# Optimization experiments

Hardware: AMD Instinct MI355X
Metric: run time of the kernel (lower is better)

Reference implementation:

```python
import jax, jax.numpy as jnp
import numpy as np

B, S, DIM = 2, 2048, 4096
NH, NKV, HD = 32, 8, 128
RANK, ALPHA = 16, 32
THETA = 500000.0
SCALE = ALPHA / RANK  # 2.0


def setup_inputs() -> dict:
    key = jax.random.key(0)
    ks = jax.random.split(key, 14)
    s = 0.02  # init scale for numerical stability
    inp = {
        "x": jax.random.normal(ks[0], (B, S, DIM), jnp.float32),
        "w_q": jax.random.normal(ks[1], (NH * HD, DIM), jnp.float32) * s,
        "w_k": jax.random.normal(ks[2], (NKV * HD, DIM), jnp.float32) * s,
        "w_v": jax.random.normal(ks[3], (NKV * HD, DIM), jnp.float32) * s,
        "w_o": jax.random.normal(ks[4], (DIM, NH * HD), jnp.float32) * s,
        "lora_wq_a": jax.random.normal(ks[5], (RANK, DIM), jnp.float32) * s,
        "lora_wq_b": jax.random.normal(ks[6], (NH * HD, RANK), jnp.float32) * s,
        "lora_wk_a": jax.random.normal(ks[7], (RANK, DIM), jnp.float32) * s,
        "lora_wk_b": jax.random.normal(ks[8], (NKV * HD, RANK), jnp.float32) * s,
        "lora_wv_a": jax.random.normal(ks[9], (RANK, DIM), jnp.float32) * s,
        "lora_wv_b": jax.random.normal(ks[10], (NKV * HD, RANK), jnp.float32) * s,
        "lora_wo_a": jax.random.normal(ks[11], (RANK, DIM), jnp.float32) * s,
        "lora_wo_b": jax.random.normal(ks[12], (DIM, RANK), jnp.float32) * s,
        "cache_k": jnp.zeros((B, S, NKV, HD), jnp.float32),
        "cache_v": jnp.zeros((B, S, NKV, HD), jnp.float32),
    }
    # rotary frequencies: freqs_cis = exp(i * t * theta^{-2j/hd}), shape (S, HD//2)
    inv_freq = 1.0 / (THETA ** (np.arange(0, HD, 2, dtype=np.float32) / HD))
    t = np.arange(S, dtype=np.float32)
    freqs = np.outer(t, inv_freq)
    inp["freqs_cos"] = jnp.asarray(np.cos(freqs))
    inp["freqs_sin"] = jnp.asarray(np.sin(freqs))
    # causal mask (prefill)
    inp["mask"] = jnp.triu(jnp.full((S, S), -1e9, jnp.float32), 1)
    inp["start_pos"] = 0
    return inp


def _apply_rope(t, cos, sin):
    # t: [b, s, h, d]; cos/sin: [s, d//2] -> complex rotation on (even, odd) pairs
    b, s, h, d = t.shape
    t2 = t.reshape(b, s, h, d // 2, 2)
    tr, ti = t2[..., 0], t2[..., 1]
    c = cos[None, :, None, :]
    sn = sin[None, :, None, :]
    out = jnp.stack([tr * c - ti * sn, tr * sn + ti * c], axis=-1)
    return out.reshape(b, s, h, d)


def reference(x, w_q, w_k, w_v, w_o,
              lora_wq_a, lora_wq_b, lora_wk_a, lora_wk_b,
              lora_wv_a, lora_wv_b, lora_wo_a, lora_wo_b,
              cache_k, cache_v, freqs_cos, freqs_sin, mask, start_pos):
    bsz, seqlen, _ = x.shape
    n_rep = NH // NKV

    xq = x @ w_q.T + SCALE * ((x @ lora_wq_a.T) @ lora_wq_b.T)
    xk = x @ w_k.T + SCALE * ((x @ lora_wk_a.T) @ lora_wk_b.T)
    xv = x @ w_v.T + SCALE * ((x @ lora_wv_a.T) @ lora_wv_b.T)

    xq = xq.reshape(bsz, seqlen, NH, HD)
    xk = xk.reshape(bsz, seqlen, NKV, HD)
    xv = xv.reshape(bsz, seqlen, NKV, HD)

    xq = _apply_rope(xq, freqs_cos, freqs_sin)
    xk = _apply_rope(xk, freqs_cos, freqs_sin)

    # KV-cache write + read of [:start_pos+seqlen]
    cache_k = jax.lax.dynamic_update_slice(cache_k, xk, (0, start_pos, 0, 0))
    cache_v = jax.lax.dynamic_update_slice(cache_v, xv, (0, start_pos, 0, 0))
    kv_len = start_pos + seqlen
    keys = cache_k[:, :kv_len]      # [b, k, nkv, hd]
    values = cache_v[:, :kv_len]

    # GQA expansion (repeat_interleave on head axis)
    keys = jnp.repeat(keys, n_rep, axis=2)    # [b, k, nh, hd]
    values = jnp.repeat(values, n_rep, axis=2)

    scores = jnp.einsum("bqhd,bkhd->bhqk", xq, keys) / jnp.sqrt(jnp.float32(HD))
    scores = scores + mask[None, None, :, :]
    probs = jax.nn.softmax(scores.astype(jnp.float32), axis=-1).astype(xq.dtype)
    out = jnp.einsum("bhqk,bkhd->bqhd", probs, values).reshape(bsz, seqlen, NH * HD)

    # NOTE: the original applies the output LoRA to x (not to out) -- kept faithful.
    return out @ w_o.T + SCALE * ((x @ lora_wo_a.T) @ lora_wo_b.T)
```

## Files before the change

### kernel.cpp

```cpp
#include <hip/hip_runtime.h>


typedef __attribute__((ext_vector_type(8))) short short8;
typedef __attribute__((ext_vector_type(4))) short short4v;
typedef __attribute__((ext_vector_type(4))) float f32x4;

#define LORA_SCALE 2.0f
#define INV_SQRT_HD 0.08838834764831845f

static __device__ __forceinline__ unsigned short f2bf(float f) {
  union { float f; unsigned int u; } v; v.f = f;
  unsigned int r = (v.u + 0x7fffu + ((v.u >> 16) & 1u)) >> 16;
  return (unsigned short)r;
}
static __device__ __forceinline__ float bf2f(unsigned short h) {
  union { unsigned int u; float f; } v; v.u = ((unsigned int)h) << 16;
  return v.f;
}

#define GL16(src, dst) __builtin_amdgcn_global_load_lds( \
    (const unsigned int __attribute__((address_space(1)))*)(src), \
    (unsigned int __attribute__((address_space(3)))*)(dst), 16, 0, 0)

#define VMC4() asm volatile("s_waitcnt vmcnt(4)" ::: "memory")
#define VMC0() asm volatile("s_waitcnt vmcnt(0)" ::: "memory")
#define BARX() __builtin_amdgcn_s_barrier()

template <int BF16OUT>
__global__ __launch_bounds__(512, 2) void gemm256_kernel(
    const unsigned short* __restrict__ A,
    const unsigned short* __restrict__ B,
    void* __restrict__ C, int K, int ldc, int T)
{
  __shared__ unsigned short As[2][2][8192];
  __shared__ unsigned short Bs[2][2][8192];
  const int tid = threadIdx.x;
  const int w = tid >> 6, l = tid & 63;
  const int l15 = l & 15, lhi = l >> 4;
  const int gx = gridDim.x;
  const int flat = blockIdx.y * gx + blockIdx.x;
  const int chunk = (gx * gridDim.y) >> 3;
  const int swz = (flat & 7) * chunk + (flat >> 3);
  const int m0 = (swz / gx) * 256, n0 = (swz % gx) * 256;
  const int wm = (w >> 2) * 128, wn = (w & 3) * 64;

  const f32x4 vz = {0.f, 0.f, 0.f, 0.f};
  f32x4 acc[8][4];
#pragma unroll
  for (int i = 0; i < 8; ++i)
#pragma unroll
    for (int j = 0; j < 4; ++j) acc[i][j] = vz;

  const int srow = tid >> 2, sg = tid & 3;
  const int sgsw = sg ^ ((tid >> 3) & 3);
  const unsigned short* gA = A + (size_t)(m0 + srow) * K + sgsw * 8;
  const unsigned short* gB = B + (size_t)(n0 + srow) * K + sgsw * 8;
  const size_t rK = (size_t)128 * K;
  const int ld0 = srow * 32 + sg * 8;

#define STAGE_A(buf, kh, kb) do { \
    GL16(gA + (kb) + (kh) * 32, &As[buf][kh][ld0]); \
    GL16(gA + rK + (kb) + (kh) * 32, &As[buf][kh][4096 + ld0]); } while (0)
#define STAGE_B(buf, kh, kb) do { \
    GL16(gB + (kb) + (kh) * 32, &Bs[buf][kh][ld0]); \
    GL16(gB + rK + (kb) + (kh) * 32, &Bs[buf][kh][4096 + ld0]); } while (0)
#define LDA8(buf, kc) do { \
    _Pragma("unroll") for (int mi = 0; mi < 8; ++mi) { \
      int r = wm + mi * 16 + l15; \
      af[mi] = *(const short8*)&As[buf][kc][r * 32 + ((lhi ^ ((r >> 1) & 3)) << 3)]; } } while (0)
#define LDB1(buf, kc, ni) \
    (*(const short8*)&Bs[buf][kc][(wn + (ni) * 16 + l15) * 32 + \
        ((lhi ^ (((wn + (ni) * 16 + l15) >> 1) & 3)) << 3)])
#define MM16(bx, by, cx, cy) do { \
    __builtin_amdgcn_s_setprio(1); \
    _Pragma("unroll") for (int mi = 0; mi < 8; ++mi) { \
      acc[mi][cx] = __builtin_amdgcn_mfma_f32_16x16x32_bf16(af[mi], bx, acc[mi][cx], 0, 0, 0); \
      acc[mi][cy] = __builtin_amdgcn_mfma_f32_16x16x32_bf16(af[mi], by, acc[mi][cy], 0, 0, 0); } \
    __builtin_amdgcn_s_setprio(0); } while (0)

  STAGE_A(0, 0, 0); STAGE_B(0, 0, 0); STAGE_A(0, 1, 0); STAGE_B(0, 1, 0);
  VMC4(); BARX();

  short8 af[8], b0, b1, b2, b3;
  for (int t = 0; t < T - 1; ++t) {
    const int cur = t & 1, nxt = cur ^ 1;
    const int kb = (t + 1) * 64;
    LDA8(cur, 0);
    b0 = LDB1(cur, 0, 0); b1 = LDB1(cur, 0, 1);
    STAGE_A(nxt, 0, kb);
    MM16(b0, b1, 0, 1);
    b2 = LDB1(cur, 0, 2); b3 = LDB1(cur, 0, 3);
    STAGE_B(nxt, 0, kb);
    VMC4(); BARX();
    MM16(b2, b3, 2, 3);
    LDA8(cur, 1);
    b0 = LDB1(cur, 1, 0); b1 = LDB1(cur, 1, 1);
    STAGE_A(nxt, 1, kb);
    MM16(b0, b1, 0, 1);
    b2 = LDB1(cur, 1, 2); b3 = LDB1(cur, 1, 3);
    STAGE_B(nxt, 1, kb);
    VMC4(); BARX();
    MM16(b2, b3, 2, 3);
  }
  {
    const int cur = (T - 1) & 1;
    LDA8(cur, 0);
    b0 = LDB1(cur, 0, 0); b1 = LDB1(cur, 0, 1);
    MM16(b0, b1, 0, 1);
    b2 = LDB1(cur, 0, 2); b3 = LDB1(cur, 0, 3);
    VMC0(); BARX();
    MM16(b2, b3, 2, 3);
    LDA8(cur, 1);
    b0 = LDB1(cur, 1, 0); b1 = LDB1(cur, 1, 1);
    MM16(b0, b1, 0, 1);
    b2 = LDB1(cur, 1, 2); b3 = LDB1(cur, 1, 3);
    MM16(b2, b3, 2, 3);
  }
#pragma unroll
  for (int mi = 0; mi < 8; ++mi)
#pragma unroll
    for (int ni = 0; ni < 4; ++ni)
#pragma unroll
      for (int j = 0; j < 4; ++j) {
        size_t row = (size_t)(m0 + wm + mi * 16 + lhi * 4 + j);
        size_t col = (size_t)(n0 + wn + ni * 16 + l15);
        if (BF16OUT) ((unsigned short*)C)[row * ldc + col] = f2bf(acc[mi][ni][j]);
        else         ((float*)C)[row * ldc + col] = acc[mi][ni][j];
      }
#undef STAGE_A
#undef STAGE_B
#undef LDA8
#undef LDB1
#undef MM16
}

template <int BF16OUT>
__global__ __launch_bounds__(512, 2) void gemm256b_kernel(
    const unsigned short* __restrict__ A,
    const unsigned short* __restrict__ B,
    void* __restrict__ C, int K, int ldc, int T)
{
  __shared__ unsigned short As[2][8192];
  __shared__ unsigned short Bs[2][8192];
  const int tid = threadIdx.x;
  const int w = tid >> 6, l = tid & 63;
  const int l15 = l & 15, lhi = l >> 4;
  const int gx = gridDim.x;
  const int flat = blockIdx.y * gx + blockIdx.x;
  const int chunk = (gx * gridDim.y) >> 3;
  const int swz = (flat & 7) * chunk + (flat >> 3);
  const int m0 = (swz / gx) * 256, n0 = (swz % gx) * 256;
  const int wm = (w >> 2) * 128, wn = (w & 3) * 64;

  const f32x4 vz = {0.f, 0.f, 0.f, 0.f};
  f32x4 acc[8][4];
#pragma unroll
  for (int i = 0; i < 8; ++i)
#pragma unroll
    for (int j = 0; j < 4; ++j) acc[i][j] = vz;

  const int srow = tid >> 2, sg = tid & 3;
  const int sgsw = sg ^ ((tid >> 3) & 3);
  const unsigned short* gA = A + (size_t)(m0 + srow) * K + sgsw * 8;
  const unsigned short* gB = B + (size_t)(n0 + srow) * K + sgsw * 8;
  const size_t rK = (size_t)128 * K;
  const int ld0 = srow * 32 + sg * 8;

#define STAGE_AB(buf, kb) do { \
    GL16(gA + (kb), &As[buf][ld0]); \
    GL16(gA + rK + (kb), &As[buf][4096 + ld0]); \
    GL16(gB + (kb), &Bs[buf][ld0]); \
    GL16(gB + rK + (kb), &Bs[buf][4096 + ld0]); } while (0)
#define LDA8(buf) do { \
    _Pragma("unroll") for (int mi = 0; mi < 8; ++mi) { \
      int r = wm + mi * 16 + l15; \
      af[mi] = *(const short8*)&As[buf][r * 32 + ((lhi ^ ((r >> 1) & 3)) << 3)]; } } while (0)
#define LDB1(buf, ni) \
    (*(const short8*)&Bs[buf][(wn + (ni) * 16 + l15) * 32 + \
        ((lhi ^ (((wn + (ni) * 16 + l15) >> 1) & 3)) << 3)])
#define MM16(bx, by, cx, cy) do { \
    __builtin_amdgcn_s_setprio(1); \
    _Pragma("unroll") for (int mi = 0; mi < 8; ++mi) { \
      acc[mi][cx] = __builtin_amdgcn_mfma_f32_16x16x32_bf16(af[mi], bx, acc[mi][cx], 0, 0, 0); \
      acc[mi][cy] = __builtin_amdgcn_mfma_f32_16x16x32_bf16(af[mi], by, acc[mi][cy], 0, 0, 0); } \
    __builtin_amdgcn_s_setprio(0); } while (0)

  STAGE_AB(0, 0);
  VMC0(); BARX();

  short8 af[8], b0, b1, b2, b3;
  for (int t = 0; t < T - 1; ++t) {
    const int cur = t & 1, nxt = cur ^ 1;
    STAGE_AB(nxt, (t + 1) * 32);
    LDA8(cur);
    b0 = LDB1(cur, 0); b1 = LDB1(cur, 1);
    MM16(b0, b1, 0, 1);
    b2 = LDB1(cur, 2); b3 = LDB1(cur, 3);
    MM16(b2, b3, 2, 3);
    VMC0(); BARX();
  }
  {
    const int cur = (T - 1) & 1;
    LDA8(cur);
    b0 = LDB1(cur, 0); b1 = LDB1(cur, 1);
    MM16(b0, b1, 0, 1);
    b2 = LDB1(cur, 2); b3 = LDB1(cur, 3);
    MM16(b2, b3, 2, 3);
  }
#pragma unroll
  for (int mi = 0; mi < 8; ++mi)
#pragma unroll
    for (int ni = 0; ni < 4; ++ni)
#pragma unroll
      for (int j = 0; j < 4; ++j) {
        size_t row = (size_t)(m0 + wm + mi * 16 + lhi * 4 + j);
        size_t col = (size_t)(n0 + wn + ni * 16 + l15);
        if (BF16OUT) ((unsigned short*)C)[row * ldc + col] = f2bf(acc[mi][ni][j]);
        else         ((float*)C)[row * ldc + col] = acc[mi][ni][j];
      }
#undef STAGE_AB
#undef LDA8
#undef LDB1
#undef MM16
}

__device__ __forceinline__ void flash_tile(
    const unsigned short* __restrict__ Ks,
    const unsigned short* __restrict__ Vt,
    unsigned short* __restrict__ Psw,
    const short8 (&qf)[2][4], f32x4 (&po)[2][8],
    float (&mrun)[2][4], float (&lrun)[2][4],
    int kv0, int qw0, int l15, int lhi)
{
  const f32x4 vzero = {0.f, 0.f, 0.f, 0.f};
  f32x4 sa[2][4];
#pragma unroll
  for (int mf = 0; mf < 2; ++mf)
#pragma unroll
    for (int nf = 0; nf < 4; ++nf) sa[mf][nf] = vzero;
  __builtin_amdgcn_s_setprio(1);
#pragma unroll
  for (int kc = 0; kc < 4; ++kc) {
    short8 kf[4];
#pragma unroll
    for (int nf = 0; nf < 4; ++nf) {
      int row = nf * 16 + l15;
      kf[nf] = *(const short8*)&Ks[row * 128 + ((kc * 32 + lhi * 8) ^ ((row & 7) << 3))];
    }
#pragma unroll
    for (int mf = 0; mf < 2; ++mf)
#pragma unroll
      for (int nf = 0; nf < 4; ++nf)
        sa[mf][nf] = __builtin_amdgcn_mfma_f32_16x16x32_bf16(qf[mf][kc], kf[nf], sa[mf][nf], 0, 0, 0);
  }
  __builtin_amdgcn_s_setprio(0);
  const bool diag = (kv0 + 63) > qw0;
#pragma unroll
  for (int mf = 0; mf < 2; ++mf) {
#pragma unroll
    for (int nf = 0; nf < 4; ++nf)
#pragma unroll
      for (int j = 0; j < 4; ++j) {
        float v = sa[mf][nf][j] * INV_SQRT_HD;
        if (diag) {
          int kvc = kv0 + nf * 16 + l15;
          int qr  = qw0 + mf * 16 + lhi * 4 + j;
          if (kvc > qr) v = -1e30f;
        }
        sa[mf][nf][j] = v;
      }
#pragma unroll
    for (int j = 0; j < 4; ++j) {
      float rm = fmaxf(fmaxf(sa[mf][0][j], sa[mf][1][j]), fmaxf(sa[mf][2][j], sa[mf][3][j]));
#pragma unroll
      for (int d = 1; d < 16; d <<= 1) rm = fmaxf(rm, __shfl_xor(rm, d));
      float mnew = fmaxf(mrun[mf][j], rm);
      float sc = __expf(mrun[mf][j] - mnew);
      float rs = 0.f;
#pragma unroll
      for (int nf = 0; nf < 4; ++nf) {
        float p = __expf(sa[mf][nf][j] - mnew);
        sa[mf][nf][j] = p;
        rs += p;
      }
#pragma unroll
      for (int d = 1; d < 16; d <<= 1) rs += __shfl_xor(rs, d);
      lrun[mf][j] = lrun[mf][j] * sc + rs;
      mrun[mf][j] = mnew;
#pragma unroll
      for (int df = 0; df < 8; ++df) po[mf][df][j] *= sc;
    }
#pragma unroll
    for (int j = 0; j < 4; ++j) {
      int q = mf * 16 + lhi * 4 + j;
      int sq = (q & 7) << 3;
#pragma unroll
      for (int nf = 0; nf < 4; ++nf)
        Psw[q * 64 + ((nf * 16 + l15) ^ sq)] = f2bf(sa[mf][nf][j]);
    }
  }
  __builtin_amdgcn_s_setprio(1);
#pragma unroll
  for (int kc2 = 0; kc2 < 2; ++kc2) {
    short8 pf[2];
#pragma unroll
    for (int mf = 0; mf < 2; ++mf) {
      int q = mf * 16 + l15;
      pf[mf] = *(const short8*)&Psw[q * 64 + ((kc2 * 32 + lhi * 8) ^ ((q & 7) << 3))];
    }
#pragma unroll
    for (int df = 0; df < 8; ++df) {
      int d = df * 16 + l15;
      int sv = ((d & 7) ^ ((d >> 3) & 7)) << 3;
      short8 vf = *(const short8*)&Vt[d * 64 + ((kc2 * 32 + lhi * 8) ^ sv)];
#pragma unroll
      for (int mf = 0; mf < 2; ++mf)
        po[mf][df] = __builtin_amdgcn_mfma_f32_16x16x32_bf16(pf[mf], vf, po[mf][df], 0, 0, 0);
    }
  }
  __builtin_amdgcn_s_setprio(0);
}

__global__ __launch_bounds__(512, 2) void flash_kernel(
    const unsigned short* __restrict__ qkv,
    unsigned short* __restrict__ outA)
{
  __shared__ unsigned short Ks[64 * 128];
  __shared__ unsigned short Vt[128 * 64];
  __shared__ unsigned short Ps[8][32 * 64];
  const int tid = threadIdx.x;
  const int w = tid >> 6, l = tid & 63;
  const int l15 = l & 15, lhi = l >> 4;
  const int h = blockIdx.y, b = blockIdx.z;
  const int p = (b == 0) ? (int)blockIdx.x : 7 - (int)blockIdx.x;
  const int qt = 2 * p + (w >> 2);
  const int qw0 = qt * 128 + (w & 3) * 32;
  const int kh = h >> 2;
  const size_t rowb = (size_t)b * 2048;

  short8 qf[2][4];
#pragma unroll
  for (int mf = 0; mf < 2; ++mf)
#pragma unroll
    for (int kc = 0; kc < 4; ++kc)
      qf[mf][kc] = *(const short8*)&qkv[(rowb + qw0 + mf * 16 + l15) * 6144 + h * 128 + kc * 32 + lhi * 8];

  const f32x4 vzero = {0.f, 0.f, 0.f, 0.f};
  f32x4 po[2][8];
  float mrun[2][4], lrun[2][4];
#pragma unroll
  for (int mf = 0; mf < 2; ++mf) {
#pragma unroll
    for (int df = 0; df < 8; ++df) po[mf][df] = vzero;
#pragma unroll
    for (int j = 0; j < 4; ++j) { mrun[mf][j] = -1e30f; lrun[mf][j] = 0.f; }
  }

  const int vrg = tid >> 4;
  const int vg  = tid & 15;

  const int nt = 2 * (2 * p + 1) + 2;
  for (int t = 0; t < nt; ++t) {
    const int kv0 = t * 64;
#pragma unroll
    for (int it = 0; it < 2; ++it) {
      int idx = it * 512 + tid;
      int r = idx >> 4, g = idx & 15;
      GL16(&qkv[(rowb + kv0 + r) * 6144 + 4096 + kh * 128 + ((g * 8) ^ ((r & 7) << 3))],
           &Ks[r * 128 + g * 8]);
    }
    if (tid < 256) {
      short8 v0, v1, v2, v3;
      const size_t vb = (rowb + kv0 + vrg * 4) * 6144 + kh * 128 + vg * 8 + 5120;
      v0 = *(const short8*)&qkv[vb];
      v1 = *(const short8*)&qkv[vb + 6144];
      v2 = *(const short8*)&qkv[vb + 12288];
      v3 = *(const short8*)&qkv[vb + 18432];
#pragma unroll
      for (int e = 0; e < 8; ++e) {
        int d = vg * 8 + e;
        int sv = ((d & 7) ^ ((d >> 3) & 7)) << 3;
        short4v o; o[0] = v0[e]; o[1] = v1[e]; o[2] = v2[e]; o[3] = v3[e];
        *(short4v*)&Vt[d * 64 + ((vrg * 4) ^ sv)] = o;
      }
    }
    __syncthreads();
    if (kv0 <= qw0 + 31)
      flash_tile(Ks, Vt, Ps[w], qf, po, mrun, lrun, kv0, qw0, l15, lhi);
    __syncthreads();
  }
#pragma unroll
  for (int mf = 0; mf < 2; ++mf)
#pragma unroll
    for (int df = 0; df < 8; ++df)
#pragma unroll
      for (int j = 0; j < 4; ++j) {
        size_t q = (size_t)(qw0 + mf * 16 + lhi * 4 + j);
        int d = df * 16 + l15;
        outA[(rowb + q) * 4160 + h * 128 + d] = f2bf(po[mf][df][j] / lrun[mf][j]);
      }
}

__global__ __launch_bounds__(256) void fold_all_kernel(
    const float* __restrict__ wq, const float* __restrict__ wk, const float* __restrict__ wv,
    const float* __restrict__ bq, const float* __restrict__ bk, const float* __restrict__ bv,
    const float* __restrict__ aq, const float* __restrict__ ak, const float* __restrict__ av,
    unsigned short* __restrict__ W)
{
  __shared__ unsigned short als[16][512];
  const int tid = threadIdx.x;
  const int ng0 = blockIdx.x * 8;
  const int c0 = blockIdx.y * 512;
  const float *wsrc, *bsrc, *asrc;
  int nl0;
  if (ng0 < 4096)      { wsrc = wq; bsrc = bq; asrc = aq; nl0 = ng0; }
  else if (ng0 < 5120) { wsrc = wk; bsrc = bk; asrc = ak; nl0 = ng0 - 4096; }
  else                 { wsrc = wv; bsrc = bv; asrc = av; nl0 = ng0 - 5120; }
#pragma unroll
  for (int it = 0; it < 8; ++it) {
    int flat = it * 1024 + tid * 4;
    int r = flat >> 9, c = flat & 511;
    f32x4 v = *(const f32x4*)&asrc[(size_t)r * 4096 + c0 + c];
    short4v o;
#pragma unroll
    for (int e = 0; e < 4; ++e) o[e] = (short)f2bf(LORA_SCALE * v[e]);
    *(short4v*)&als[r][c] = o;
  }
  __syncthreads();
  const int nr = tid >> 5;
  const int cb = (tid & 31) * 16;
  const float* wrow = wsrc + (size_t)(nl0 + nr) * 4096 + c0 + cb;
  const float* brow = bsrc + (size_t)(nl0 + nr) * 16;
  float bb[16];
#pragma unroll
  for (int r4 = 0; r4 < 4; ++r4) {
    f32x4 t = *(const f32x4*)&brow[r4 * 4];
#pragma unroll
    for (int e = 0; e < 4; ++e) bb[r4 * 4 + e] = t[e];
  }
  float acc[16];
#pragma unroll
  for (int j4 = 0; j4 < 4; ++j4) {
    f32x4 t = *(const f32x4*)&wrow[j4 * 4];
#pragma unroll
    for (int e = 0; e < 4; ++e) acc[j4 * 4 + e] = t[e];
  }
#pragma unroll
  for (int r = 0; r < 16; ++r) {
    short8 a0 = *(const short8*)&als[r][cb];
    short8 a1 = *(const short8*)&als[r][cb + 8];
    float br = bb[r];
#pragma unroll
    for (int e = 0; e < 8; ++e) {
      acc[e]     += br * bf2f((unsigned short)a0[e]);
      acc[8 + e] += br * bf2f((unsigned short)a1[e]);
    }
  }
  short8 o0, o1;
#pragma unroll
  for (int e = 0; e < 8; ++e) { o0[e] = (short)f2bf(acc[e]); o1[e] = (short)f2bf(acc[8 + e]); }
  unsigned short* dst = W + (size_t)(ng0 + nr) * 4096 + c0 + cb;
  *(short8*)&dst[0] = o0;
  *(short8*)&dst[8] = o1;
}

__global__ void build_wo_kernel(const float* __restrict__ wo, const float* __restrict__ bo,
                                unsigned short* __restrict__ W)
{
  int idx = blockIdx.x * 256 + threadIdx.x;
  int n = idx / 520;
  int c8 = (idx - n * 520) * 8;
  short8 o;
  if (c8 < 4096) {
    const float* src = wo + (size_t)n * 4096 + c8;
    f32x4 a = *(const f32x4*)&src[0];
    f32x4 b2 = *(const f32x4*)&src[4];
#pragma unroll
    for (int e = 0; e < 4; ++e) { o[e] = (short)f2bf(a[e]); o[4 + e] = (short)f2bf(b2[e]); }
  } else {
#pragma unroll
    for (int e = 0; e < 8; ++e) {
      int j = c8 + e - 4096;
      float v = (j < 16) ? bo[(size_t)n * 16 + j] : 0.f;
      o[e] = (short)f2bf(v);
    }
  }
  *(short8*)&W[(size_t)n * 4160 + c8] = o;
}

__global__ __launch_bounds__(256) void convert_t_kernel(
    const float* __restrict__ x, const float* __restrict__ ao,
    unsigned short* __restrict__ Xb, unsigned short* __restrict__ Ao)
{
  __shared__ float red[4][16];
  const int m = blockIdx.x;
  const int tid = threadIdx.x;
  const int w = tid >> 6, l = tid & 63;
  float part[16];
#pragma unroll
  for (int r = 0; r < 16; ++r) part[r] = 0.f;
#pragma unroll
  for (int it = 0; it < 4; ++it) {
    int k = it * 1024 + tid * 4;
    f32x4 xv = *(const f32x4*)&x[(size_t)m * 4096 + k];
    short4v o;
#pragma unroll
    for (int e = 0; e < 4; ++e) o[e] = (short)f2bf(xv[e]);
    *(short4v*)&Xb[(size_t)m * 4096 + k] = o;
#pragma unroll
    for (int r = 0; r < 16; ++r) {
      f32x4 av = *(const f32x4*)&ao[(size_t)r * 4096 + k];
      part[r] += xv[0] * av[0] + xv[1] * av[1] + xv[2] * av[2] + xv[3] * av[3];
    }
  }
#pragma unroll
  for (int d = 1; d < 64; d <<= 1)
#pragma unroll
    for (int r = 0; r < 16; ++r) part[r] += __shfl_xor(part[r], d);
  if (l == 0)
#pragma unroll
    for (int r = 0; r < 16; ++r) red[w][r] = part[r];
  __syncthreads();
  if (tid < 64) {
    float v = 0.f;
    if (tid < 16) v = LORA_SCALE * (red[0][tid] + red[1][tid] + red[2][tid] + red[3][tid]);
    Ao[(size_t)m * 4160 + 4096 + tid] = f2bf(v);
  }
}

__global__ void rope_kernel(unsigned short* __restrict__ qkv,
                            const float* __restrict__ fcos,
                            const float* __restrict__ fsin)
{
  int idx = blockIdx.x * 256 + threadIdx.x;
  int m = idx / 640;
  int c8 = (idx - m * 640) * 8;
  int s = m & 2047;
  int i0 = (c8 & 127) >> 1;
  unsigned short* p = qkv + (size_t)m * 6144 + c8;
  short8 v = *(short8*)p;
  f32x4 c = *(const f32x4*)&fcos[s * 64 + i0];
  f32x4 sn = *(const f32x4*)&fsin[s * 64 + i0];
  short8 o;
#pragma unroll
  for (int pr = 0; pr < 4; ++pr) {
    float re = bf2f((unsigned short)v[2 * pr]);
    float im = bf2f((unsigned short)v[2 * pr + 1]);
    o[2 * pr]     = (short)f2bf(re * c[pr] - im * sn[pr]);
    o[2 * pr + 1] = (short)f2bf(re * sn[pr] + im * c[pr]);
  }
  *(short8*)p = o;
}

extern "C" void kernel_launch(void* const* d_in, const int* in_sizes, int n_in,
                              void* d_out, int out_size, void* d_ws, size_t ws_size,
                              hipStream_t stream) {
  (void)in_sizes; (void)n_in; (void)out_size; (void)ws_size;
  const float* x    = (const float*)d_in[0];
  const float* w_q  = (const float*)d_in[1];
  const float* w_k  = (const float*)d_in[2];
  const float* w_v  = (const float*)d_in[3];
  const float* w_o  = (const float*)d_in[4];
  const float* la_q = (const float*)d_in[5];
  const float* lb_q = (const float*)d_in[6];
  const float* la_k = (const float*)d_in[7];
  const float* lb_k = (const float*)d_in[8];
  const float* la_v = (const float*)d_in[9];
  const float* lb_v = (const float*)d_in[10];
  const float* la_o = (const float*)d_in[11];
  const float* lb_o = (const float*)d_in[12];
  const float* fcos = (const float*)d_in[15];
  const float* fsin = (const float*)d_in[16];

  unsigned short* Wqkv = (unsigned short*)d_ws;
  unsigned short* Wo   = Wqkv + (size_t)6144 * 4096;
  unsigned short* Xbf  = Wo + (size_t)4096 * 4160;
  unsigned short* QKV  = Xbf + (size_t)4096 * 4096;
  unsigned short* Ao   = QKV + (size_t)4096 * 6144;

  dim3 blk(256);
  fold_all_kernel<<<dim3(768, 8), blk, 0, stream>>>(
      w_q, w_k, w_v, lb_q, lb_k, lb_v, la_q, la_k, la_v, Wqkv);
  build_wo_kernel<<<8320, blk, 0, stream>>>(w_o, lb_o, Wo);
  convert_t_kernel<<<4096, blk, 0, stream>>>(x, la_o, Xbf, Ao);
  gemm256b_kernel<1><<<dim3(24, 16), dim3(512), 0, stream>>>(Xbf, Wqkv, QKV, 4096, 6144, 128);
  rope_kernel<<<10240, blk, 0, stream>>>(QKV, fcos, fsin);
  flash_kernel<<<dim3(8, 32, 2), dim3(512), 0, stream>>>(QKV, Ao);
  gemm256_kernel<0><<<dim3(16, 16), dim3(512), 0, stream>>>(Ao, Wo, d_out, 4160, 4096, 65);
}
```

Baseline: 715.0 us.

## Split QKV projection into 256x256 Q GEMM and 128x256 KV GEMM

Splits the fused QKV projection into two launches. The Q part (N=4096) reuses the deeper-pipelined 256x256 kernel with a K step of 64. The KV part (N=2048) goes to a new 128x256-tile kernel with K=64 double buffering and finer-grained barrier and vmcnt interleaving. The aim is better occupancy and load/MFMA overlap than the old 24x16 grid of 256x256 tiles with a 32-wide K step. The cost is an extra kernel launch and the loss of the grid swizzle in the new kernel.

```diff
diff --git a/kernel.cpp b/kernel.cpp
--- a/kernel.cpp
+++ b/kernel.cpp
@@ -22,6 +22,7 @@
     (const unsigned int __attribute__((address_space(1)))*)(src), \
     (unsigned int __attribute__((address_space(3)))*)(dst), 16, 0, 0)
 
+#define VMC3() asm volatile("s_waitcnt vmcnt(3)" ::: "memory")
 #define VMC4() asm volatile("s_waitcnt vmcnt(4)" ::: "memory")
 #define VMC0() asm volatile("s_waitcnt vmcnt(0)" ::: "memory")
 #define BARX() __builtin_amdgcn_s_barrier()
@@ -135,27 +136,23 @@
 }
 
 template <int BF16OUT>
-__global__ __launch_bounds__(512, 2) void gemm256b_kernel(
+__global__ __launch_bounds__(512, 2) void gemm128_kernel(
     const unsigned short* __restrict__ A,
     const unsigned short* __restrict__ B,
     void* __restrict__ C, int K, int ldc, int T)
 {
-  __shared__ unsigned short As[2][8192];
-  __shared__ unsigned short Bs[2][8192];
+  __shared__ unsigned short As[2][2][4096];
+  __shared__ unsigned short Bs[2][2][8192];
   const int tid = threadIdx.x;
   const int w = tid >> 6, l = tid & 63;
   const int l15 = l & 15, lhi = l >> 4;
-  const int gx = gridDim.x;
-  const int flat = blockIdx.y * gx + blockIdx.x;
-  const int chunk = (gx * gridDim.y) >> 3;
-  const int swz = (flat & 7) * chunk + (flat >> 3);
-  const int m0 = (swz / gx) * 256, n0 = (swz % gx) * 256;
-  const int wm = (w >> 2) * 128, wn = (w & 3) * 64;
+  const int m0 = blockIdx.y * 128, n0 = blockIdx.x * 256;
+  const int wm = (w >> 2) * 64, wn = (w & 3) * 64;
 
   const f32x4 vz = {0.f, 0.f, 0.f, 0.f};
-  f32x4 acc[8][4];
-#pragma unroll
-  for (int i = 0; i < 8; ++i)
+  f32x4 acc[4][4];
+#pragma unroll
+  for (int i = 0; i < 4; ++i)
 #pragma unroll
     for (int j = 0; j < 4; ++j) acc[i][j] = vz;
 
@@ -166,49 +163,68 @@
   const size_t rK = (size_t)128 * K;
   const int ld0 = srow * 32 + sg * 8;
 
-#define STAGE_AB(buf, kb) do { \
-    GL16(gA + (kb), &As[buf][ld0]); \
-    GL16(gA + rK + (kb), &As[buf][4096 + ld0]); \
-    GL16(gB + (kb), &Bs[buf][ld0]); \
-    GL16(gB + rK + (kb), &Bs[buf][4096 + ld0]); } while (0)
-#define LDA8(buf) do { \
-    _Pragma("unroll") for (int mi = 0; mi < 8; ++mi) { \
+#define STAGE_A(buf, kh, kb) \
+    GL16(gA + (kb) + (kh) * 32, &As[buf][kh][ld0])
+#define STAGE_B(buf, kh, kb) do { \
+    GL16(gB + (kb) + (kh) * 32, &Bs[buf][kh][ld0]); \
+    GL16(gB + rK + (kb) + (kh) * 32, &Bs[buf][kh][4096 + ld0]); } while (0)
+#define LDA4(buf, kc) do { \
+    _Pragma("unroll") for (int mi = 0; mi < 4; ++mi) { \
       int r = wm + mi * 16 + l15; \
-      af[mi] = *(const short8*)&As[buf][r * 32 + ((lhi ^ ((r >> 1) & 3)) << 3)]; } } while (0)
-#define LDB1(buf, ni) \
-    (*(const short8*)&Bs[buf][(wn + (ni) * 16 + l15) * 32 + \
+      af[mi] = *(const short8*)&As[buf][kc][r * 32 + ((lhi ^ ((r >> 1) & 3)) << 3)]; } } while (0)
+#define LDB1(buf, kc, ni) \
+    (*(const short8*)&Bs[buf][kc][(wn + (ni) * 16 + l15) * 32 + \
         ((lhi ^ (((wn + (ni) * 16 + l15) >> 1) & 3)) << 3)])
-#define MM16(bx, by, cx, cy) do { \
+#define MM8(bx, by, cx, cy) do { \
     __builtin_amdgcn_s_setprio(1); \
-    _Pragma("unroll") for (int mi = 0; mi < 8; ++mi) { \
+    _Pragma("unroll") for (int mi = 0; mi < 4; ++mi) { \
       acc[mi][cx] = __builtin_amdgcn_mfma_f32_16x16x32_bf16(af[mi], bx, acc[mi][cx], 0, 0, 0); \
       acc[mi][cy] = __builtin_amdgcn_mfma_f32_16x16x32_bf16(af[mi], by, acc[mi][cy], 0, 0, 0); } \
     __builtin_amdgcn_s_setprio(0); } while (0)
 
-  STAGE_AB(0, 0);
-  VMC0(); BARX();
-
-  short8 af[8], b0, b1, b2, b3;
+  STAGE_A(0, 0, 0); STAGE_B(0, 0, 0); STAGE_A(0, 1, 0); STAGE_B(0, 1, 0);
+  VMC3(); BARX();
+
+  short8 af[4], b0, b1, b2, b3;
   for (int t = 0; t < T - 1; ++t) {
     const int cur = t & 1, nxt = cur ^ 1;
-    STAGE_AB(nxt, (t + 1) * 32);
-    LDA8(cur);
-    b0 = LDB1(cur, 0); b1 = LDB1(cur, 1);
-    MM16(b0, b1, 0, 1);
-    b2 = LDB1(cur, 2); b3 = LDB1(cur, 3);
-    MM16(b2, b3, 2, 3);
-    VMC0(); BARX();
+    const int kb = (t + 1) * 64;
+    LDA4(cur, 0);
+    b0 = LDB1(cur, 0, 0); b1 = LDB1(cur, 0, 1);
+    STAGE_A(nxt, 0, kb);
+    BARX();
+    MM8(b0, b1, 0, 1);
+    b2 = LDB1(cur, 0, 2); b3 = LDB1(cur, 0, 3);
+    STAGE_B(nxt, 0, kb);
+    VMC3(); BARX();
+    MM8(b2, b3, 2, 3);
+    LDA4(cur, 1);
+    b0 = LDB1(cur, 1, 0); b1 = LDB1(cur, 1, 1);
+    STAGE_A(nxt, 1, kb);
+    BARX();
+    MM8(b0, b1, 0, 1);
+    b2 = LDB1(cur, 1, 2); b3 = LDB1(cur, 1, 3);
+    STAGE_B(nxt, 1, kb);
+    VMC3(); BARX();
+    MM8(b2, b3, 2, 3);
   }
   {
     const int cur = (T - 1) & 1;
-    LDA8(cur);
-    b0 = LDB1(cur, 0); b1 = LDB1(cur, 1);
-    MM16(b0, b1, 0, 1);
-    b2 = LDB1(cur, 2); b3 = LDB1(cur, 3);
-    MM16(b2, b3, 2, 3);
-  }
-#pragma unroll
-  for (int mi = 0; mi < 8; ++mi)
+    LDA4(cur, 0);
+    b0 = LDB1(cur, 0, 0); b1 = LDB1(cur, 0, 1);
+    BARX();
+    MM8(b0, b1, 0, 1);
+    b2 = LDB1(cur, 0, 2); b3 = LDB1(cur, 0, 3);
+    VMC0(); BARX();
+    MM8(b2, b3, 2, 3);
+    LDA4(cur, 1);
+    b0 = LDB1(cur, 1, 0); b1 = LDB1(cur, 1, 1);
+    MM8(b0, b1, 0, 1);
+    b2 = LDB1(cur, 1, 2); b3 = LDB1(cur, 1, 3);
+    MM8(b2, b3, 2, 3);
+  }
+#pragma unroll
+  for (int mi = 0; mi < 4; ++mi)
 #pragma unroll
     for (int ni = 0; ni < 4; ++ni)
 #pragma unroll
@@ -218,10 +234,11 @@
         if (BF16OUT) ((unsigned short*)C)[row * ldc + col] = f2bf(acc[mi][ni][j]);
         else         ((float*)C)[row * ldc + col] = acc[mi][ni][j];
       }
-#undef STAGE_AB
-#undef LDA8
+#undef STAGE_A
+#undef STAGE_B
+#undef LDA4
 #undef LDB1
-#undef MM16
+#undef MM8
 }
 
 __device__ __forceinline__ void flash_tile(
@@ -583,7 +600,9 @@
       w_q, w_k, w_v, lb_q, lb_k, lb_v, la_q, la_k, la_v, Wqkv);
   build_wo_kernel<<<8320, blk, 0, stream>>>(w_o, lb_o, Wo);
   convert_t_kernel<<<4096, blk, 0, stream>>>(x, la_o, Xbf, Ao);
-  gemm256b_kernel<1><<<dim3(24, 16), dim3(512), 0, stream>>>(Xbf, Wqkv, QKV, 4096, 6144, 128);
+  gemm256_kernel<1><<<dim3(16, 16), dim3(512), 0, stream>>>(Xbf, Wqkv, QKV, 4096, 6144, 64);
+  gemm128_kernel<1><<<dim3(8, 32), dim3(512), 0, stream>>>(
+      Xbf, Wqkv + (size_t)4096 * 4096, QKV + 4096, 4096, 6144, 64);
   rope_kernel<<<10240, blk, 0, stream>>>(QKV, fcos, fsin);
   flash_kernel<<<dim3(8, 32, 2), dim3(512), 0, stream>>>(QKV, Ao);
   gemm256_kernel<0><<<dim3(16, 16), dim3(512), 0, stream>>>(Ao, Wo, d_out, 4160, 4096, 65);
```

Measured after the change: 639.0 us. -10.6%, faster.
